# Kernel optimization log

Hardware: AMD Instinct MI355X
Metric: run time of the kernel (lower is better)

The kernel has to match this reference:

```python
import jax, jax.numpy as jnp
import numpy as np

EPS_MIN = 1e-8
EPS_MAX = 1.0


def setup_inputs() -> dict:
    key = jax.random.key(0)
    k0, k1, k2, k3 = jax.random.split(key, 4)
    B, H, NT, NV = 8, 16, 512, 576
    return {
        "attn_t_0": jax.random.uniform(k0, (B, H, NT, NV), dtype=jnp.float32),
        "attn_v_0": jax.random.uniform(k1, (B, H, NV, NT), dtype=jnp.float32),
        "attn_t_1": jax.random.uniform(k2, (B, H, NT, NV), dtype=jnp.float32),
        "attn_v_1": jax.random.uniform(k3, (B, H, NV, NT), dtype=jnp.float32),
    }


def _layer_loss(attn_t, attn_v):
    # Head-mean attention maps
    P_t = attn_t.mean(axis=1)  # (B, NT, NV)
    P_v = attn_v.mean(axis=1)  # (B, NV, NT)
    # Only the diagonals of P_t @ P_v and P_v @ P_t are used:
    # diag(A @ B)[b, i] = sum_k A[b, i, k] * B[b, k, i]
    text_diag = jnp.einsum('bik,bki->bi', P_t, P_v)    # (B, NT)
    vision_diag = jnp.einsum('bjk,bkj->bj', P_v, P_t)  # (B, NV)
    text_diag = jnp.clip(text_diag, EPS_MIN, EPS_MAX)
    vision_diag = jnp.clip(vision_diag, EPS_MIN, EPS_MAX)
    loss_text = -jnp.log(text_diag).mean()
    loss_vision = -jnp.log(vision_diag).mean()
    return (loss_text + loss_vision) * 0.5


def reference(attn_t_0, attn_v_0, attn_t_1, attn_v_1) -> jnp.ndarray:
    layers = [(attn_t_0, attn_v_0), (attn_t_1, attn_v_1)]
    total = jnp.float32(0.0)
    for at, av in layers:
        total = total + _layer_loss(at, av)
    return total / len(layers)
```

## Files before the change

kernel.cpp:

```cpp
#include <hip/hip_runtime.h>
#include <math.h>

constexpr int B  = 8;
constexpr int H  = 16;
constexpr int NT = 512;
constexpr int NV = 576;
constexpr int TILE = 64;
constexpr float INV_H2 = 1.0f / (float)(H * H);

constexpr int TEXT_N = 2 * B * NT;
constexpr int VIS_N  = 2 * B * NV;

__global__ void zero_ws_kernel(float* __restrict__ ws, int n) {
    int i = blockIdx.x * blockDim.x + threadIdx.x;
    if (i < n) ws[i] = 0.0f;
}

__global__ __launch_bounds__(256) void fused_diag_kernel(
    const float* __restrict__ t0, const float* __restrict__ v0,
    const float* __restrict__ t1, const float* __restrict__ v1,
    float* __restrict__ text_acc,
    float* __restrict__ vis_acc)
{
    const int ktile = blockIdx.x;
    const int itile = blockIdx.y;
    const int bz    = blockIdx.z;
    const int b     = bz & (B - 1);
    const int layer = bz >> 3;

    const float* __restrict__ T = layer ? t1 : t0;
    const float* __restrict__ V = layer ? v1 : v0;

    const int tid = threadIdx.x;
    const int c = tid & 15;
    const int g = tid >> 4;

    const int i0 = itile * TILE;
    const int k0 = ktile * TILE;

    const size_t tbase = (size_t)b * H * NT * NV + (size_t)i0 * NV + k0;
    const size_t vbase = (size_t)b * H * NV * NT + (size_t)k0 * NT + i0;

    float4 tacc[4];
    float4 vacc[4];
#pragma unroll
    for (int r = 0; r < 4; ++r) {
        tacc[r] = make_float4(0.f, 0.f, 0.f, 0.f);
        vacc[r] = make_float4(0.f, 0.f, 0.f, 0.f);
    }

    for (int h = 0; h < H; ++h) {
        const float* tp = T + tbase + (size_t)h * NT * NV;
        const float* vp = V + vbase + (size_t)h * NV * NT;
#pragma unroll
        for (int r = 0; r < 4; ++r) {
            const int row = g + 16 * r;
            const float4 tv = *(const float4*)(tp + (size_t)row * NV + 4 * c);
            const float4 vv = *(const float4*)(vp + (size_t)row * NT + 4 * c);
            tacc[r].x += tv.x; tacc[r].y += tv.y; tacc[r].z += tv.z; tacc[r].w += tv.w;
            vacc[r].x += vv.x; vacc[r].y += vv.y; vacc[r].z += vv.z; vacc[r].w += vv.w;
        }
    }

    __shared__ float vlds[TILE * 65];
    __shared__ float rowsum[TILE];
    __shared__ float colsum[TILE];

    if (tid < TILE) {
        rowsum[tid] = 0.0f;
        colsum[tid] = 0.0f;
    }

#pragma unroll
    for (int r = 0; r < 4; ++r) {
        const int kk = g + 16 * r;
        float* p = &vlds[kk * 65 + 4 * c];
        p[0] = vacc[r].x; p[1] = vacc[r].y; p[2] = vacc[r].z; p[3] = vacc[r].w;
    }
    __syncthreads();

    float colpart[4] = {0.f, 0.f, 0.f, 0.f};
#pragma unroll
    for (int r = 0; r < 4; ++r) {
        const int ii = g + 16 * r;
        const float tq[4] = {tacc[r].x, tacc[r].y, tacc[r].z, tacc[r].w};
        float rp = 0.f;
#pragma unroll
        for (int j = 0; j < 4; ++j) {
            const int kk = 4 * c + j;
            const float q = tq[j] * vlds[kk * 65 + ii];
            rp += q;
            colpart[j] += q;
        }
        atomicAdd(&rowsum[ii], rp);
    }
#pragma unroll
    for (int j = 0; j < 4; ++j) {
        atomicAdd(&colsum[4 * c + j], colpart[j]);
    }
    __syncthreads();

    const int lb = layer * B + b;
    if (tid < TILE) {
        atomicAdd(&text_acc[(size_t)lb * NT + i0 + tid], rowsum[tid] * INV_H2);
    } else if (tid < 2 * TILE) {
        const int kk = tid - TILE;
        atomicAdd(&vis_acc[(size_t)lb * NV + k0 + kk], colsum[kk] * INV_H2);
    }
}

__global__ __launch_bounds__(256) void finalize_kernel(
    const float* __restrict__ text_acc,
    const float* __restrict__ vis_acc,
    float* __restrict__ out)
{
    const int tid = threadIdx.x;
    const float wt = 0.25f / (float)(B * NT);
    const float wv = 0.25f / (float)(B * NV);

    float s = 0.f;
    for (int i = tid; i < TEXT_N; i += 256) {
        float x = text_acc[i];
        x = fminf(fmaxf(x, 1e-8f), 1.0f);
        s += -logf(x) * wt;
    }
    for (int i = tid; i < VIS_N; i += 256) {
        float x = vis_acc[i];
        x = fminf(fmaxf(x, 1e-8f), 1.0f);
        s += -logf(x) * wv;
    }

#pragma unroll
    for (int off = 32; off > 0; off >>= 1) s += __shfl_down(s, off, 64);

    __shared__ float wsum[4];
    if ((tid & 63) == 0) wsum[tid >> 6] = s;
    __syncthreads();
    if (tid == 0) out[0] = wsum[0] + wsum[1] + wsum[2] + wsum[3];
}

extern "C" void kernel_launch(void* const* d_in, const int* in_sizes, int n_in,
                              void* d_out, int out_size, void* d_ws, size_t ws_size,
                              hipStream_t stream) {
    const float* t0 = (const float*)d_in[0];
    const float* v0 = (const float*)d_in[1];
    const float* t1 = (const float*)d_in[2];
    const float* v1 = (const float*)d_in[3];

    float* text_acc = (float*)d_ws;
    float* vis_acc  = text_acc + TEXT_N;
    float* out      = (float*)d_out;

    {
        const int n = TEXT_N + VIS_N;
        zero_ws_kernel<<<(n + 255) / 256, 256, 0, stream>>>(text_acc, n);
    }

    {
        dim3 grid(NV / TILE, NT / TILE, 2 * B);
        fused_diag_kernel<<<grid, 256, 0, stream>>>(t0, v0, t1, v1, text_acc, vis_acc);
    }

    finalize_kernel<<<1, 256, 0, stream>>>(text_acc, vis_acc, out);
}
```

Measured before the change: 504.1 us.

## Split head reduction into streaming headsum kernel before diag computation

Adds a separate kernel that sums attention maps over heads with fully contiguous float4 streaming, writing head-summed maps to workspace, followed by a diag kernel reading those maps. This replaces the fused kernel's strided per-tile head loop, which had poor access locality, with a coalesced streaming pass. It adds an extra write and read of the head-summed maps plus one kernel launch, and falls back to the fused path if the workspace is too small.

```diff
diff --git a/kernel.cpp b/kernel.cpp
--- a/kernel.cpp
+++ b/kernel.cpp
@@ -8,12 +8,120 @@
 constexpr int TILE = 64;
 constexpr float INV_H2 = 1.0f / (float)(H * H);
 
+constexpr int MN  = NT * NV;
+constexpr int MN4 = MN / 4;
+constexpr int W4  = B * MN4;
+constexpr int TOTAL4 = 4 * W4;
+
 constexpr int TEXT_N = 2 * B * NT;
 constexpr int VIS_N  = 2 * B * NV;
 
 __global__ void zero_ws_kernel(float* __restrict__ ws, int n) {
     int i = blockIdx.x * blockDim.x + threadIdx.x;
     if (i < n) ws[i] = 0.0f;
+}
+
+__global__ __launch_bounds__(256) void headsum_kernel(
+    const float* __restrict__ t0, const float* __restrict__ v0,
+    const float* __restrict__ t1, const float* __restrict__ v1,
+    float4* __restrict__ S4)
+{
+    const int idx = blockIdx.x * 256 + threadIdx.x;
+    if (idx >= TOTAL4) return;
+
+    const int tsel = idx / W4;
+    const int rem  = idx - tsel * W4;
+    const float* src = (tsel == 0) ? t0 : (tsel == 1) ? v0
+                     : (tsel == 2) ? t1 : v1;
+    const int b  = rem / MN4;
+    const int p4 = rem - b * MN4;
+
+    const float4* p = (const float4*)src + (size_t)b * (H * MN4) + p4;
+
+    float4 acc = make_float4(0.f, 0.f, 0.f, 0.f);
+#pragma unroll
+    for (int h = 0; h < H; ++h) {
+        const float4 x = p[(size_t)h * MN4];
+        acc.x += x.x; acc.y += x.y; acc.z += x.z; acc.w += x.w;
+    }
+    S4[idx] = acc;
+}
+
+__global__ __launch_bounds__(256) void diag_kernel(
+    const float* __restrict__ S,
+    float* __restrict__ text_acc,
+    float* __restrict__ vis_acc)
+{
+    const int ktile = blockIdx.x;
+    const int itile = blockIdx.y;
+    const int bz    = blockIdx.z;
+    const int b     = bz & (B - 1);
+    const int layer = bz >> 3;
+
+    const float* __restrict__ St = S + ((size_t)(2 * layer)     * B + b) * MN;
+    const float* __restrict__ Sv = S + ((size_t)(2 * layer + 1) * B + b) * MN;
+
+    const int tid = threadIdx.x;
+    const int c = tid & 15;
+    const int g = tid >> 4;
+
+    const int i0 = itile * TILE;
+    const int k0 = ktile * TILE;
+
+    float4 tacc[4];
+    float4 vacc[4];
+#pragma unroll
+    for (int r = 0; r < 4; ++r) {
+        const int row = g + 16 * r;
+        tacc[r] = *(const float4*)(St + (size_t)(i0 + row) * NV + k0 + 4 * c);
+        vacc[r] = *(const float4*)(Sv + (size_t)(k0 + row) * NT + i0 + 4 * c);
+    }
+
+    __shared__ float vlds[TILE * 65];
+    __shared__ float rowsum[TILE];
+    __shared__ float colsum[TILE];
+
+    if (tid < TILE) {
+        rowsum[tid] = 0.0f;
+        colsum[tid] = 0.0f;
+    }
+
+#pragma unroll
+    for (int r = 0; r < 4; ++r) {
+        const int kk = g + 16 * r;
+        float* p = &vlds[kk * 65 + 4 * c];
+        p[0] = vacc[r].x; p[1] = vacc[r].y; p[2] = vacc[r].z; p[3] = vacc[r].w;
+    }
+    __syncthreads();
+
+    float colpart[4] = {0.f, 0.f, 0.f, 0.f};
+#pragma unroll
+    for (int r = 0; r < 4; ++r) {
+        const int ii = g + 16 * r;
+        const float tq[4] = {tacc[r].x, tacc[r].y, tacc[r].z, tacc[r].w};
+        float rp = 0.f;
+#pragma unroll
+        for (int j = 0; j < 4; ++j) {
+            const int kk = 4 * c + j;
+            const float q = tq[j] * vlds[kk * 65 + ii];
+            rp += q;
+            colpart[j] += q;
+        }
+        atomicAdd(&rowsum[ii], rp);
+    }
+#pragma unroll
+    for (int j = 0; j < 4; ++j) {
+        atomicAdd(&colsum[4 * c + j], colpart[j]);
+    }
+    __syncthreads();
+
+    const int lb = layer * B + b;
+    if (tid < TILE) {
+        atomicAdd(&text_acc[(size_t)lb * NT + i0 + tid], rowsum[tid] * INV_H2);
+    } else if (tid < 2 * TILE) {
+        const int kk = tid - TILE;
+        atomicAdd(&vis_acc[(size_t)lb * NV + k0 + kk], colsum[kk] * INV_H2);
+    }
 }
 
 __global__ __launch_bounds__(256) void fused_diag_kernel(
@@ -146,20 +254,38 @@
     const float* v0 = (const float*)d_in[1];
     const float* t1 = (const float*)d_in[2];
     const float* v1 = (const float*)d_in[3];
-
-    float* text_acc = (float*)d_ws;
-    float* vis_acc  = text_acc + TEXT_N;
-    float* out      = (float*)d_out;
-
-    {
-        const int n = TEXT_N + VIS_N;
-        zero_ws_kernel<<<(n + 255) / 256, 256, 0, stream>>>(text_acc, n);
-    }
-
-    {
-        dim3 grid(NV / TILE, NT / TILE, 2 * B);
-        fused_diag_kernel<<<grid, 256, 0, stream>>>(t0, v0, t1, v1, text_acc, vis_acc);
-    }
-
-    finalize_kernel<<<1, 256, 0, stream>>>(text_acc, vis_acc, out);
-}
+    float* out = (float*)d_out;
+
+    constexpr size_t S_FLOATS = (size_t)4 * B * MN;
+    constexpr size_t NEED = (S_FLOATS + TEXT_N + VIS_N) * sizeof(float);
+
+    if (ws_size >= NEED) {
+        float* S        = (float*)d_ws;
+        float* text_acc = S + S_FLOATS;
+        float* vis_acc  = text_acc + TEXT_N;
+
+        {
+            const int n = TEXT_N + VIS_N;
+            zero_ws_kernel<<<(n + 255) / 256, 256, 0, stream>>>(text_acc, n);
+        }
+        headsum_kernel<<<TOTAL4 / 256, 256, 0, stream>>>(t0, v0, t1, v1, (float4*)S);
+        {
+            dim3 grid(NV / TILE, NT / TILE, 2 * B);
+            diag_kernel<<<grid, 256, 0, stream>>>(S, text_acc, vis_acc);
+        }
+        finalize_kernel<<<1, 256, 0, stream>>>(text_acc, vis_acc, out);
+    } else {
+        float* text_acc = (float*)d_ws;
+        float* vis_acc  = text_acc + TEXT_N;
+
+        {
+            const int n = TEXT_N + VIS_N;
+            zero_ws_kernel<<<(n + 255) / 256, 256, 0, stream>>>(text_acc, n);
+        }
+        {
+            dim3 grid(NV / TILE, NT / TILE, 2 * B);
+            fused_diag_kernel<<<grid, 256, 0, stream>>>(t0, v0, t1, v1, text_acc, vis_acc);
+        }
+        finalize_kernel<<<1, 256, 0, stream>>>(text_acc, vis_acc, out);
+    }
+}
```

Result: slower. 515.9 us (+2.3%).
